# Optimization experiments

Measured on AMD Instinct MI355X. Metric: run time of the kernel, lower is better.

The kernel has to match this reference:

```python
import jax, jax.numpy as jnp
import numpy as np

N_SRC = 50000
N_DST = 50000
E = 800000
IN_DIM = 128
OUT_DIM = 64
HEADS = 4
NEG_SLOPE = 0.2  # PyG GATConv default negative_slope
EPS = 1e-16      # PyG softmax denominator epsilon


def setup_inputs() -> dict:
    key = jax.random.key(0)
    ks = jax.random.split(key, 8)
    x_src = jax.random.normal(ks[0], (N_SRC, IN_DIM), dtype=jnp.float32)
    x_dst = jax.random.normal(ks[1], (N_DST, IN_DIM), dtype=jnp.float32)
    src = jax.random.randint(ks[2], (E,), 0, N_SRC, dtype=jnp.int32)
    dst = jax.random.randint(ks[3], (E,), 0, N_DST, dtype=jnp.int32)
    edge_index = jnp.stack([src, dst], axis=0)
    W_src = jax.random.normal(ks[4], (IN_DIM, HEADS * OUT_DIM), dtype=jnp.float32) / np.sqrt(IN_DIM)
    W_dst = jax.random.normal(ks[5], (IN_DIM, HEADS * OUT_DIM), dtype=jnp.float32) / np.sqrt(IN_DIM)
    att_src = jax.random.normal(ks[6], (HEADS, OUT_DIM), dtype=jnp.float32) / np.sqrt(OUT_DIM)
    att_dst = jax.random.normal(ks[7], (HEADS, OUT_DIM), dtype=jnp.float32) / np.sqrt(OUT_DIM)
    bias = jnp.zeros((OUT_DIM,), dtype=jnp.float32)
    return {"x_src": x_src, "x_dst": x_dst, "edge_index": edge_index,
            "W_src": W_src, "W_dst": W_dst, "att_src": att_src,
            "att_dst": att_dst, "bias": bias}


def reference(x_src, x_dst, edge_index, W_src, W_dst, att_src, att_dst, bias):
    # Linear projections -> [N, H, C]
    hs = (x_src @ W_src).reshape(N_SRC, HEADS, OUT_DIM)
    hd = (x_dst @ W_dst).reshape(N_DST, HEADS, OUT_DIM)
    # Per-node attention logits -> [N, H]
    a_s = jnp.einsum('nhc,hc->nh', hs, att_src)
    a_d = jnp.einsum('nhc,hc->nh', hd, att_dst)

    src, dst = edge_index[0], edge_index[1]
    # Per-edge logits [E, H]
    alpha = jax.nn.leaky_relu(a_s[src] + a_d[dst], negative_slope=NEG_SLOPE)
    # Segment softmax over edges sharing the same dst node
    amax = jax.ops.segment_max(alpha, dst, num_segments=N_DST)
    alpha = jnp.exp(alpha - amax[dst])
    denom = jax.ops.segment_sum(alpha, dst, num_segments=N_DST)
    alpha = alpha / (denom[dst] + EPS)
    # (dropout=0 / eval mode: no attention dropout)
    # Message + scatter-add aggregation: out[i] = sum_e alpha_e * hs[src_e]
    msg = hs[src] * alpha[:, :, None]                 # [E, H, C]
    out = jax.ops.segment_sum(msg, dst, num_segments=N_DST)  # [N_dst, H, C]
    # concat=False -> mean over heads, then bias
    return out.mean(axis=1) + bias
```

## Files before the change

### kernel.cpp

```cpp
#include <hip/hip_runtime.h>
#include <hip/hip_bf16.h>

#define N_SRC 50000
#define N_DST 50000
#define NEDGE 800000
#define IND   128
#define HEADS 4
#define CDIM  64
#define HC    256
#define KTOT  512
#define MAXDEG 96
#define HIST_GPB 256
#define NB_HIST2 2048
#define DPG 6250
#define NB_G16 3125
#define NB_CAST 3125

typedef _Float16 half8  __attribute__((ext_vector_type(8)));
typedef _Float16 half2t __attribute__((ext_vector_type(2)));
typedef float    f32x4  __attribute__((ext_vector_type(4)));
typedef int      i32x4  __attribute__((ext_vector_type(4)));

static __device__ __forceinline__ unsigned int pack2h(float a, float b) {
    union { half2t h; unsigned int u; } v;
    v.h[0] = (_Float16)a; v.h[1] = (_Float16)b;
    return v.u;
}
static __device__ __forceinline__ half2t bits2h(unsigned int u) {
    union { unsigned int u; half2t h; } v; v.u = u; return v.h;
}

__global__ void prep0_kernel(const float* __restrict__ Wdst,
                             const float* __restrict__ att_d,
                             float* __restrict__ WdA,
                             const float* __restrict__ Wsrc,
                             const float* __restrict__ att_s,
                             float* __restrict__ WsA,
                             _Float16* __restrict__ WfT,
                             int* __restrict__ deg) {
    int b = blockIdx.x, tid = threadIdx.x;
    if (b < 196) {
        int i = b * 256 + tid;
        if (i < N_DST) deg[i] = 0;
    } else if (b < 198) {
        int id = (b - 196) * 256 + tid;
        int k = id >> 2, h = id & 3;
        float acc = 0.f;
        for (int c = 0; c < CDIM; ++c)
            acc += Wdst[k * HC + h * CDIM + c] * att_d[h * CDIM + c];
        WdA[id] = acc;
    } else if (b < 200) {
        int id = (b - 198) * 256 + tid;
        int k = id >> 2, h = id & 3;
        float acc = 0.f;
        for (int c = 0; c < CDIM; ++c)
            acc += Wsrc[k * HC + h * CDIM + c] * att_s[h * CDIM + c];
        WsA[id] = acc;
    } else {
        int idx = (b - 200) * 256 + tid;
        int c = idx >> 9, hk = idx & 511;
        int h = hk >> 7, k = hk & 127;
        WfT[idx] = (_Float16)Wsrc[k * HC + h * CDIM + c];
    }
}

__global__ __launch_bounds__(256) void big_kernel(
        const float* __restrict__ x_dst, const float* __restrict__ WdA,
        float* __restrict__ a_d,
        const float* __restrict__ x_src, const float* __restrict__ WsA,
        float* __restrict__ a_s,
        _Float16* __restrict__ xh,
        const int* __restrict__ src, const int* __restrict__ dst,
        int* __restrict__ deg, int* __restrict__ col2) {
    int b = blockIdx.x, tid = threadIdx.x;
    if (b < NB_HIST2) {
        int g  = b & 7;
        int bg = b >> 3;
        int lo = g * DPG, hi = lo + DPG;
        #pragma unroll 1
        for (int it = 0; it < 4; ++it) {
            int base = ((it * HIST_GPB + bg) << 10) + (tid << 2);
            if (base >= NEDGE) break;
            i32x4 dv = __builtin_nontemporal_load((const i32x4*)(dst + base));
            i32x4 sv = __builtin_nontemporal_load((const i32x4*)(src + base));
            #pragma unroll
            for (int j = 0; j < 4; ++j) {
                int d = dv[j];
                if (d >= lo && d < hi) {
                    int r = atomicAdd(&deg[d], 1);
                    if (r < MAXDEG) col2[d * MAXDEG + r] = sv[j];
                }
            }
        }
        return;
    }
    int rank = b - NB_HIST2;
    if (rank < 2 * NB_G16) {
        const float* xbase; const float4* wa; float* outp; int which;
        if (rank < NB_G16) { xbase = x_dst; wa = (const float4*)WdA; outp = a_d; which = rank; }
        else               { xbase = x_src; wa = (const float4*)WsA; outp = a_s; which = rank - NB_G16; }
        int w = tid >> 6, lane = tid & 63;
        float4 wa0 = wa[lane], wa1 = wa[lane + 64];
        int n0 = which * 16 + w * 4;
        #pragma unroll
        for (int p = 0; p < 4; ++p) {
            int n = n0 + p;
            const float* xp = xbase + (size_t)n * IND;
            float x0 = xp[lane], x1 = xp[lane + 64];
            float p0 = x0 * wa0.x + x1 * wa1.x;
            float p1 = x0 * wa0.y + x1 * wa1.y;
            float p2 = x0 * wa0.z + x1 * wa1.z;
            float p3 = x0 * wa0.w + x1 * wa1.w;
            for (int off = 32; off >= 1; off >>= 1) {
                p0 += __shfl_xor(p0, off, 64);
                p1 += __shfl_xor(p1, off, 64);
                p2 += __shfl_xor(p2, off, 64);
                p3 += __shfl_xor(p3, off, 64);
            }
            if (lane == 0) {
                outp[n * 4 + 0] = p0; outp[n * 4 + 1] = p1;
                outp[n * 4 + 2] = p2; outp[n * 4 + 3] = p3;
            }
        }
    } else {
        int e = (rank - 2 * NB_G16) * 256 + tid;
        const float* xp = x_src + (size_t)e * 8;
        float4 u0 = *(const float4*)(xp);
        float4 u1 = *(const float4*)(xp + 4);
        half8 v;
        v[0] = (_Float16)u0.x; v[1] = (_Float16)u0.y;
        v[2] = (_Float16)u0.z; v[3] = (_Float16)u0.w;
        v[4] = (_Float16)u1.x; v[5] = (_Float16)u1.y;
        v[6] = (_Float16)u1.z; v[7] = (_Float16)u1.w;
        *(half8*)(xh + (size_t)e * 8) = v;
    }
}

__global__ __launch_bounds__(256) void aggregate_kernel(
        const int* __restrict__ deg, const int* __restrict__ col2,
        const float4* __restrict__ as4, const float4* __restrict__ ad4,
        const unsigned int* __restrict__ xh32,
        unsigned int* __restrict__ z32) {
    __shared__ int    s_off[4][MAXDEG];
    __shared__ float4 s_w[4][MAXDEG];
    int tid = threadIdx.x;
    int wv = tid >> 6, lane = tid & 63;
    int i = (blockIdx.x * 256 + tid) >> 6;
    if (i >= N_DST) return;
    int dg = deg[i]; if (dg > MAXDEG) dg = MAXDEG;
    unsigned int* zo = z32 + (size_t)i * 256 + lane;
    if (dg == 0) {
        zo[0] = 0u; zo[64] = 0u; zo[128] = 0u; zo[192] = 0u;
        return;
    }
    float4 ad = ad4[i];
    const int* crow = col2 + i * MAXDEG;

    float s0 = 0.f, s1 = 0.f, s2 = 0.f, s3 = 0.f;
    for (int e = lane; e < dg; e += 64) {
        int sn = crow[e];
        float4 av = as4[sn];
        float lx = av.x + ad.x; lx = lx > 0.f ? lx : 0.2f * lx;
        float ly = av.y + ad.y; ly = ly > 0.f ? ly : 0.2f * ly;
        float lz = av.z + ad.z; lz = lz > 0.f ? lz : 0.2f * lz;
        float lw = av.w + ad.w; lw = lw > 0.f ? lw : 0.2f * lw;
        float w0 = __expf(lx), w1 = __expf(ly), w2 = __expf(lz), w3 = __expf(lw);
        s0 += w0; s1 += w1; s2 += w2; s3 += w3;
        s_off[wv][e] = sn;
        s_w[wv][e] = (float4){w0, w1, w2, w3};
    }
    for (int off = 32; off >= 1; off >>= 1) {
        s0 += __shfl_xor(s0, off, 64);
        s1 += __shfl_xor(s1, off, 64);
        s2 += __shfl_xor(s2, off, 64);
        s3 += __shfl_xor(s3, off, 64);
    }
    float i0 = 0.25f / (s0 + 1e-16f);
    float i1 = 0.25f / (s1 + 1e-16f);
    float i2 = 0.25f / (s2 + 1e-16f);
    float i3 = 0.25f / (s3 + 1e-16f);

    for (int e = lane; e < dg; e += 64) {
        float4 wf = s_w[wv][e];
        wf.x *= i0; wf.y *= i1; wf.z *= i2; wf.w *= i3;
        s_w[wv][e] = wf;
    }
    __asm__ volatile("s_waitcnt lgkmcnt(0)" ::: "memory");

    const unsigned int* xb = xh32 + lane;
    float z00 = 0.f, z01 = 0.f, z10 = 0.f, z11 = 0.f;
    float z20 = 0.f, z21 = 0.f, z30 = 0.f, z31 = 0.f;
    int j = 0;
    for (; j + 4 <= dg; j += 4) {
        int sn0 = s_off[wv][j],     sn1 = s_off[wv][j + 1];
        int sn2 = s_off[wv][j + 2], sn3 = s_off[wv][j + 3];
        float4 w0 = s_w[wv][j],     w1 = s_w[wv][j + 1];
        float4 w2 = s_w[wv][j + 2], w3 = s_w[wv][j + 3];
        unsigned int g0 = xb[sn0 << 6];
        unsigned int g1 = xb[sn1 << 6];
        unsigned int g2 = xb[sn2 << 6];
        unsigned int g3 = xb[sn3 << 6];
        half2t hx;
        hx = bits2h(g0);
        { float xa = (float)hx[0], xb2 = (float)hx[1];
          z00 += w0.x * xa; z01 += w0.x * xb2; z10 += w0.y * xa; z11 += w0.y * xb2;
          z20 += w0.z * xa; z21 += w0.z * xb2; z30 += w0.w * xa; z31 += w0.w * xb2; }
        hx = bits2h(g1);
        { float xa = (float)hx[0], xb2 = (float)hx[1];
          z00 += w1.x * xa; z01 += w1.x * xb2; z10 += w1.y * xa; z11 += w1.y * xb2;
          z20 += w1.z * xa; z21 += w1.z * xb2; z30 += w1.w * xa; z31 += w1.w * xb2; }
        hx = bits2h(g2);
        { float xa = (float)hx[0], xb2 = (float)hx[1];
          z00 += w2.x * xa; z01 += w2.x * xb2; z10 += w2.y * xa; z11 += w2.y * xb2;
          z20 += w2.z * xa; z21 += w2.z * xb2; z30 += w2.w * xa; z31 += w2.w * xb2; }
        hx = bits2h(g3);
        { float xa = (float)hx[0], xb2 = (float)hx[1];
          z00 += w3.x * xa; z01 += w3.x * xb2; z10 += w3.y * xa; z11 += w3.y * xb2;
          z20 += w3.z * xa; z21 += w3.z * xb2; z30 += w3.w * xa; z31 += w3.w * xb2; }
    }
    for (; j < dg; ++j) {
        int sn0 = s_off[wv][j];
        float4 w0 = s_w[wv][j];
        unsigned int g0 = xb[sn0 << 6];
        half2t hx = bits2h(g0);
        float xa = (float)hx[0], xb2 = (float)hx[1];
        z00 += w0.x * xa; z01 += w0.x * xb2; z10 += w0.y * xa; z11 += w0.y * xb2;
        z20 += w0.z * xa; z21 += w0.z * xb2; z30 += w0.w * xa; z31 += w0.w * xb2;
    }
    zo[0]   = pack2h(z00, z01);
    zo[64]  = pack2h(z10, z11);
    zo[128] = pack2h(z20, z21);
    zo[192] = pack2h(z30, z31);
}

__global__ __launch_bounds__(256) void fgemm_kernel(
        const _Float16* __restrict__ z, const _Float16* __restrict__ WfT,
        const float* __restrict__ bias, float* __restrict__ out) {
    __shared__ _Float16 sW[64 * KTOT];
    int tid = threadIdx.x;
    {
        const float4* wsrc = (const float4*)WfT;
        #pragma unroll
        for (int it = 0; it < 16; ++it) {
            int idx = it * 256 + tid;
            int row = idx >> 6, slot = idx & 63;
            float4 v = wsrc[idx];
            int byte_off = row * 1024 + ((slot * 16) ^ ((row & 7) << 4));
            *(float4*)((char*)sW + byte_off) = v;
        }
    }

    int w = tid >> 6, lane = tid & 63;
    int ll = lane & 15, q = lane >> 4;
    int rbase = blockIdx.x * 64 + w * 16;

    int arow = rbase + ll;
    if (arow >= N_DST) arow = N_DST - 1;
    const _Float16* zr = z + (size_t)arow * KTOT + q * 8;
    half8 afrag[16];
    #pragma unroll
    for (int s = 0; s < 16; ++s)
        afrag[s] = *(const half8*)(zr + s * 32);

    f32x4 acc[4];
    #pragma unroll
    for (int t = 0; t < 4; ++t) acc[t] = (f32x4){0.f, 0.f, 0.f, 0.f};

    __syncthreads();
    int sw = (ll & 7) << 4;
    #pragma unroll
    for (int t = 0; t < 4; ++t) {
        const char* rowp = (const char*)sW + (t * 16 + ll) * 1024;
        f32x4 c = acc[t];
        #pragma unroll
        for (int s = 0; s < 16; ++s) {
            half8 bb = *(const half8*)(rowp + ((s * 64 + q * 16) ^ sw));
            c = __builtin_amdgcn_mfma_f32_16x16x32_f16(afrag[s], bb, c, 0, 0, 0);
        }
        acc[t] = c;
    }

    #pragma unroll
    for (int t = 0; t < 4; ++t) {
        float bv = bias[t * 16 + ll];
        #pragma unroll
        for (int r = 0; r < 4; ++r) {
            int n = rbase + q * 4 + r;
            if (n < N_DST) out[(size_t)n * CDIM + t * 16 + ll] = acc[t][r] + bv;
        }
    }
}

extern "C" void kernel_launch(void* const* d_in, const int* in_sizes, int n_in,
                              void* d_out, int out_size, void* d_ws, size_t ws_size,
                              hipStream_t stream) {
    const float* x_src   = (const float*)d_in[0];
    const float* x_dst   = (const float*)d_in[1];
    const int*   ei      = (const int*)d_in[2];
    const float* W_src   = (const float*)d_in[3];
    const float* W_dst   = (const float*)d_in[4];
    const float* att_src = (const float*)d_in[5];
    const float* att_dst = (const float*)d_in[6];
    const float* bias    = (const float*)d_in[7];
    float* out = (float*)d_out;

    char* ws = (char*)d_ws;
    _Float16* xh   = (_Float16*)ws; ws += (size_t)N_SRC * IND * 2;
    _Float16* z    = (_Float16*)ws; ws += (size_t)N_DST * KTOT * 2;
    int*    col2   = (int*)ws;    ws += (size_t)N_DST * MAXDEG * 4;
    float*  a_s    = (float*)ws;  ws += (size_t)N_SRC * 4 * 4;
    float*  a_d    = (float*)ws;  ws += (size_t)N_DST * 4 * 4;
    float*  WdA    = (float*)ws;  ws += 2048;
    float*  WsA    = (float*)ws;  ws += 2048;
    _Float16* WfT  = (_Float16*)ws; ws += (size_t)CDIM * KTOT * 2;
    int*    deg    = (int*)ws;    ws += N_DST * 4;

    prep0_kernel<<<328, 256, 0, stream>>>(W_dst, att_dst, WdA,
                                          W_src, att_src, WsA, WfT, deg);
    big_kernel<<<NB_HIST2 + 2 * NB_G16 + NB_CAST, 256, 0, stream>>>(
            x_dst, WdA, a_d, x_src, WsA, a_s, xh,
            ei, ei + NEDGE, deg, col2);
    aggregate_kernel<<<(N_DST + 3) / 4, 256, 0, stream>>>(
            deg, col2, (const float4*)a_s, (const float4*)a_d,
            (const unsigned int*)xh, (unsigned int*)z);
    fgemm_kernel<<<(N_DST + 63) / 64, 256, 0, stream>>>(z, WfT, bias, out);
}
```

Before: 218.2 us.

## Fuse aggregation and final projection GEMM into one kernel via LDS staging

Merges the aggregate and fgemm kernels into one 1024-thread-block kernel. Each of 16 waves aggregates one destination row into a swizzled LDS tile, then 4 waves run the MFMA projection against the weight matrix, which is staged through LDS in two halves. This removes the global round-trip of the fp16 intermediate z (about 51MB written and read) and one kernel launch. In exchange, each block reloads the 64KB weight matrix for only 16 rows, adds several block-wide barriers, and leaves 12 of 16 waves idle during the GEMM phase.

```diff
diff --git a/kernel.cpp b/kernel.cpp
--- a/kernel.cpp
+++ b/kernel.cpp
@@ -15,6 +15,7 @@
 #define DPG 6250
 #define NB_G16 3125
 #define NB_CAST 3125
+#define NB_FUSED 3125
 
 typedef _Float16 half8  __attribute__((ext_vector_type(8)));
 typedef _Float16 half2t __attribute__((ext_vector_type(2)));
@@ -136,157 +137,144 @@
     }
 }
 
-__global__ __launch_bounds__(256) void aggregate_kernel(
+__global__ __launch_bounds__(1024, 4) void aggf_kernel(
         const int* __restrict__ deg, const int* __restrict__ col2,
         const float4* __restrict__ as4, const float4* __restrict__ ad4,
         const unsigned int* __restrict__ xh32,
-        unsigned int* __restrict__ z32) {
-    __shared__ int    s_off[4][MAXDEG];
-    __shared__ float4 s_w[4][MAXDEG];
+        const _Float16* __restrict__ WfT,
+        const float* __restrict__ bias, float* __restrict__ out) {
+    __shared__ char smem[32768];
+    __shared__ char zmem[16384];
+    int* s_off   = (int*)smem;
+    float4* s_w  = (float4*)(smem + 6144);
     int tid = threadIdx.x;
     int wv = tid >> 6, lane = tid & 63;
-    int i = (blockIdx.x * 256 + tid) >> 6;
-    if (i >= N_DST) return;
+    int i = blockIdx.x * 16 + wv;
     int dg = deg[i]; if (dg > MAXDEG) dg = MAXDEG;
-    unsigned int* zo = z32 + (size_t)i * 256 + lane;
+    char* zrow = zmem + wv * 1024;
+    int zswz = (wv & 7) << 4;
+
     if (dg == 0) {
-        zo[0] = 0u; zo[64] = 0u; zo[128] = 0u; zo[192] = 0u;
-        return;
-    }
-    float4 ad = ad4[i];
-    const int* crow = col2 + i * MAXDEG;
-
-    float s0 = 0.f, s1 = 0.f, s2 = 0.f, s3 = 0.f;
-    for (int e = lane; e < dg; e += 64) {
-        int sn = crow[e];
-        float4 av = as4[sn];
-        float lx = av.x + ad.x; lx = lx > 0.f ? lx : 0.2f * lx;
-        float ly = av.y + ad.y; ly = ly > 0.f ? ly : 0.2f * ly;
-        float lz = av.z + ad.z; lz = lz > 0.f ? lz : 0.2f * lz;
-        float lw = av.w + ad.w; lw = lw > 0.f ? lw : 0.2f * lw;
-        float w0 = __expf(lx), w1 = __expf(ly), w2 = __expf(lz), w3 = __expf(lw);
-        s0 += w0; s1 += w1; s2 += w2; s3 += w3;
-        s_off[wv][e] = sn;
-        s_w[wv][e] = (float4){w0, w1, w2, w3};
-    }
-    for (int off = 32; off >= 1; off >>= 1) {
-        s0 += __shfl_xor(s0, off, 64);
-        s1 += __shfl_xor(s1, off, 64);
-        s2 += __shfl_xor(s2, off, 64);
-        s3 += __shfl_xor(s3, off, 64);
-    }
-    float i0 = 0.25f / (s0 + 1e-16f);
-    float i1 = 0.25f / (s1 + 1e-16f);
-    float i2 = 0.25f / (s2 + 1e-16f);
-    float i3 = 0.25f / (s3 + 1e-16f);
-
-    for (int e = lane; e < dg; e += 64) {
-        float4 wf = s_w[wv][e];
-        wf.x *= i0; wf.y *= i1; wf.z *= i2; wf.w *= i3;
-        s_w[wv][e] = wf;
-    }
-    __asm__ volatile("s_waitcnt lgkmcnt(0)" ::: "memory");
-
-    const unsigned int* xb = xh32 + lane;
-    float z00 = 0.f, z01 = 0.f, z10 = 0.f, z11 = 0.f;
-    float z20 = 0.f, z21 = 0.f, z30 = 0.f, z31 = 0.f;
-    int j = 0;
-    for (; j + 4 <= dg; j += 4) {
-        int sn0 = s_off[wv][j],     sn1 = s_off[wv][j + 1];
-        int sn2 = s_off[wv][j + 2], sn3 = s_off[wv][j + 3];
-        float4 w0 = s_w[wv][j],     w1 = s_w[wv][j + 1];
-        float4 w2 = s_w[wv][j + 2], w3 = s_w[wv][j + 3];
-        unsigned int g0 = xb[sn0 << 6];
-        unsigned int g1 = xb[sn1 << 6];
-        unsigned int g2 = xb[sn2 << 6];
-        unsigned int g3 = xb[sn3 << 6];
-        half2t hx;
-        hx = bits2h(g0);
-        { float xa = (float)hx[0], xb2 = (float)hx[1];
-          z00 += w0.x * xa; z01 += w0.x * xb2; z10 += w0.y * xa; z11 += w0.y * xb2;
-          z20 += w0.z * xa; z21 += w0.z * xb2; z30 += w0.w * xa; z31 += w0.w * xb2; }
-        hx = bits2h(g1);
-        { float xa = (float)hx[0], xb2 = (float)hx[1];
-          z00 += w1.x * xa; z01 += w1.x * xb2; z10 += w1.y * xa; z11 += w1.y * xb2;
-          z20 += w1.z * xa; z21 += w1.z * xb2; z30 += w1.w * xa; z31 += w1.w * xb2; }
-        hx = bits2h(g2);
-        { float xa = (float)hx[0], xb2 = (float)hx[1];
-          z00 += w2.x * xa; z01 += w2.x * xb2; z10 += w2.y * xa; z11 += w2.y * xb2;
-          z20 += w2.z * xa; z21 += w2.z * xb2; z30 += w2.w * xa; z31 += w2.w * xb2; }
-        hx = bits2h(g3);
-        { float xa = (float)hx[0], xb2 = (float)hx[1];
-          z00 += w3.x * xa; z01 += w3.x * xb2; z10 += w3.y * xa; z11 += w3.y * xb2;
-          z20 += w3.z * xa; z21 += w3.z * xb2; z30 += w3.w * xa; z31 += w3.w * xb2; }
-    }
-    for (; j < dg; ++j) {
-        int sn0 = s_off[wv][j];
-        float4 w0 = s_w[wv][j];
-        unsigned int g0 = xb[sn0 << 6];
-        half2t hx = bits2h(g0);
-        float xa = (float)hx[0], xb2 = (float)hx[1];
-        z00 += w0.x * xa; z01 += w0.x * xb2; z10 += w0.y * xa; z11 += w0.y * xb2;
-        z20 += w0.z * xa; z21 += w0.z * xb2; z30 += w0.w * xa; z31 += w0.w * xb2;
-    }
-    zo[0]   = pack2h(z00, z01);
-    zo[64]  = pack2h(z10, z11);
-    zo[128] = pack2h(z20, z21);
-    zo[192] = pack2h(z30, z31);
-}
-
-__global__ __launch_bounds__(256) void fgemm_kernel(
-        const _Float16* __restrict__ z, const _Float16* __restrict__ WfT,
-        const float* __restrict__ bias, float* __restrict__ out) {
-    __shared__ _Float16 sW[64 * KTOT];
-    int tid = threadIdx.x;
-    {
-        const float4* wsrc = (const float4*)WfT;
+        *(unsigned int*)(zrow + (((0 * 64 + lane) * 4) ^ zswz)) = 0u;
+        *(unsigned int*)(zrow + (((1 * 64 + lane) * 4) ^ zswz)) = 0u;
+        *(unsigned int*)(zrow + (((2 * 64 + lane) * 4) ^ zswz)) = 0u;
+        *(unsigned int*)(zrow + (((3 * 64 + lane) * 4) ^ zswz)) = 0u;
+    } else {
+        float4 ad = ad4[i];
+        const int* crow = col2 + i * MAXDEG;
+
+        float s0 = 0.f, s1 = 0.f, s2 = 0.f, s3 = 0.f;
+        for (int e = lane; e < dg; e += 64) {
+            int sn = crow[e];
+            float4 av = as4[sn];
+            float lx = av.x + ad.x; lx = lx > 0.f ? lx : 0.2f * lx;
+            float ly = av.y + ad.y; ly = ly > 0.f ? ly : 0.2f * ly;
+            float lz = av.z + ad.z; lz = lz > 0.f ? lz : 0.2f * lz;
+            float lw = av.w + ad.w; lw = lw > 0.f ? lw : 0.2f * lw;
+            float w0 = __expf(lx), w1 = __expf(ly), w2 = __expf(lz), w3 = __expf(lw);
+            s0 += w0; s1 += w1; s2 += w2; s3 += w3;
+            s_off[wv * MAXDEG + e] = sn;
+            s_w[wv * MAXDEG + e] = (float4){w0, w1, w2, w3};
+        }
+        for (int off = 32; off >= 1; off >>= 1) {
+            s0 += __shfl_xor(s0, off, 64);
+            s1 += __shfl_xor(s1, off, 64);
+            s2 += __shfl_xor(s2, off, 64);
+            s3 += __shfl_xor(s3, off, 64);
+        }
+        float i0 = 0.25f / (s0 + 1e-16f);
+        float i1 = 0.25f / (s1 + 1e-16f);
+        float i2 = 0.25f / (s2 + 1e-16f);
+        float i3 = 0.25f / (s3 + 1e-16f);
+        for (int e = lane; e < dg; e += 64) {
+            float4 wf = s_w[wv * MAXDEG + e];
+            wf.x *= i0; wf.y *= i1; wf.z *= i2; wf.w *= i3;
+            s_w[wv * MAXDEG + e] = wf;
+        }
+        __asm__ volatile("s_waitcnt lgkmcnt(0)" ::: "memory");
+
+        const unsigned int* xb = xh32 + lane;
+        float z00 = 0.f, z01 = 0.f, z10 = 0.f, z11 = 0.f;
+        float z20 = 0.f, z21 = 0.f, z30 = 0.f, z31 = 0.f;
+        int j = 0;
+        for (; j + 4 <= dg; j += 4) {
+            int sn0 = s_off[wv * MAXDEG + j],     sn1 = s_off[wv * MAXDEG + j + 1];
+            int sn2 = s_off[wv * MAXDEG + j + 2], sn3 = s_off[wv * MAXDEG + j + 3];
+            float4 w0 = s_w[wv * MAXDEG + j],     w1 = s_w[wv * MAXDEG + j + 1];
+            float4 w2 = s_w[wv * MAXDEG + j + 2], w3 = s_w[wv * MAXDEG + j + 3];
+            unsigned int g0 = xb[sn0 << 6];
+            unsigned int g1 = xb[sn1 << 6];
+            unsigned int g2 = xb[sn2 << 6];
+            unsigned int g3 = xb[sn3 << 6];
+            half2t hx;
+            hx = bits2h(g0);
+            { float xa = (float)hx[0], xc = (float)hx[1];
+              z00 += w0.x * xa; z01 += w0.x * xc; z10 += w0.y * xa; z11 += w0.y * xc;
+              z20 += w0.z * xa; z21 += w0.z * xc; z30 += w0.w * xa; z31 += w0.w * xc; }
+            hx = bits2h(g1);
+            { float xa = (float)hx[0], xc = (float)hx[1];
+              z00 += w1.x * xa; z01 += w1.x * xc; z10 += w1.y * xa; z11 += w1.y * xc;
+              z20 += w1.z * xa; z21 += w1.z * xc; z30 += w1.w * xa; z31 += w1.w * xc; }
+            hx = bits2h(g2);
+            { float xa = (float)hx[0], xc = (float)hx[1];
+              z00 += w2.x * xa; z01 += w2.x * xc; z10 += w2.y * xa; z11 += w2.y * xc;
+              z20 += w2.z * xa; z21 += w2.z * xc; z30 += w2.w * xa; z31 += w2.w * xc; }
+            hx = bits2h(g3);
+            { float xa = (float)hx[0], xc = (float)hx[1];
+              z00 += w3.x * xa; z01 += w3.x * xc; z10 += w3.y * xa; z11 += w3.y * xc;
+              z20 += w3.z * xa; z21 += w3.z * xc; z30 += w3.w * xa; z31 += w3.w * xc; }
+        }
+        for (; j < dg; ++j) {
+            int sn0 = s_off[wv * MAXDEG + j];
+            float4 w0 = s_w[wv * MAXDEG + j];
+            unsigned int g0 = xb[sn0 << 6];
+            half2t hx = bits2h(g0);
+            float xa = (float)hx[0], xc = (float)hx[1];
+            z00 += w0.x * xa; z01 += w0.x * xc; z10 += w0.y * xa; z11 += w0.y * xc;
+            z20 += w0.z * xa; z21 += w0.z * xc; z30 += w0.w * xa; z31 += w0.w * xc;
+        }
+        *(unsigned int*)(zrow + (((0 * 64 + lane) * 4) ^ zswz)) = pack2h(z00, z01);
+        *(unsigned int*)(zrow + (((1 * 64 + lane) * 4) ^ zswz)) = pack2h(z10, z11);
+        *(unsigned int*)(zrow + (((2 * 64 + lane) * 4) ^ zswz)) = pack2h(z20, z21);
+        *(unsigned int*)(zrow + (((3 * 64 + lane) * 4) ^ zswz)) = pack2h(z30, z31);
+    }
+    __syncthreads();
+
+    int ll = lane & 15, q = lane >> 4;
+    int t = wv & 3;
+    int sw = (ll & 7) << 4;
+    f32x4 acc = (f32x4){0.f, 0.f, 0.f, 0.f};
+    const float4* wsrc = (const float4*)WfT;
+    #pragma unroll
+    for (int half = 0; half < 2; ++half) {
         #pragma unroll
-        for (int it = 0; it < 16; ++it) {
-            int idx = it * 256 + tid;
-            int row = idx >> 6, slot = idx & 63;
-            float4 v = wsrc[idx];
-            int byte_off = row * 1024 + ((slot * 16) ^ ((row & 7) << 4));
-            *(float4*)((char*)sW + byte_off) = v;
-        }
-    }
-
-    int w = tid >> 6, lane = tid & 63;
-    int ll = lane & 15, q = lane >> 4;
-    int rbase = blockIdx.x * 64 + w * 16;
-
-    int arow = rbase + ll;
-    if (arow >= N_DST) arow = N_DST - 1;
-    const _Float16* zr = z + (size_t)arow * KTOT + q * 8;
-    half8 afrag[16];
-    #pragma unroll
-    for (int s = 0; s < 16; ++s)
-        afrag[s] = *(const half8*)(zr + s * 32);
-
-    f32x4 acc[4];
-    #pragma unroll
-    for (int t = 0; t < 4; ++t) acc[t] = (f32x4){0.f, 0.f, 0.f, 0.f};
-
-    __syncthreads();
-    int sw = (ll & 7) << 4;
-    #pragma unroll
-    for (int t = 0; t < 4; ++t) {
-        const char* rowp = (const char*)sW + (t * 16 + ll) * 1024;
-        f32x4 c = acc[t];
-        #pragma unroll
-        for (int s = 0; s < 16; ++s) {
-            half8 bb = *(const half8*)(rowp + ((s * 64 + q * 16) ^ sw));
-            c = __builtin_amdgcn_mfma_f32_16x16x32_f16(afrag[s], bb, c, 0, 0, 0);
-        }
-        acc[t] = c;
-    }
-
-    #pragma unroll
-    for (int t = 0; t < 4; ++t) {
+        for (int it = 0; it < 2; ++it) {
+            int idx = it * 1024 + tid;
+            int row = idx >> 5, slot = idx & 31;
+            float4 v = wsrc[row * 64 + half * 32 + slot];
+            *(float4*)(smem + row * 512 + ((slot * 16) ^ ((row & 7) << 4))) = v;
+        }
+        __syncthreads();
+        if (wv < 4) {
+            const char* rowp  = smem + (t * 16 + ll) * 512;
+            const char* zbase = zmem + ll * 1024;
+            #pragma unroll
+            for (int s2 = 0; s2 < 8; ++s2) {
+                int s = half * 8 + s2;
+                half8 a  = *(const half8*)(zbase + ((s * 64 + q * 16) ^ sw));
+                half8 bb = *(const half8*)(rowp + ((s2 * 64 + q * 16) ^ sw));
+                acc = __builtin_amdgcn_mfma_f32_16x16x32_f16(a, bb, acc, 0, 0, 0);
+            }
+        }
+        __syncthreads();
+    }
+    if (wv < 4) {
         float bv = bias[t * 16 + ll];
+        int rbase = blockIdx.x * 16;
         #pragma unroll
         for (int r = 0; r < 4; ++r) {
             int n = rbase + q * 4 + r;
-            if (n < N_DST) out[(size_t)n * CDIM + t * 16 + ll] = acc[t][r] + bv;
+            out[(size_t)n * CDIM + t * 16 + ll] = acc[r] + bv;
         }
     }
 }
@@ -306,7 +294,6 @@
 
     char* ws = (char*)d_ws;
     _Float16* xh   = (_Float16*)ws; ws += (size_t)N_SRC * IND * 2;
-    _Float16* z    = (_Float16*)ws; ws += (size_t)N_DST * KTOT * 2;
     int*    col2   = (int*)ws;    ws += (size_t)N_DST * MAXDEG * 4;
     float*  a_s    = (float*)ws;  ws += (size_t)N_SRC * 4 * 4;
     float*  a_d    = (float*)ws;  ws += (size_t)N_DST * 4 * 4;
@@ -320,8 +307,7 @@
     big_kernel<<<NB_HIST2 + 2 * NB_G16 + NB_CAST, 256, 0, stream>>>(
             x_dst, WdA, a_d, x_src, WsA, a_s, xh,
             ei, ei + NEDGE, deg, col2);
-    aggregate_kernel<<<(N_DST + 3) / 4, 256, 0, stream>>>(
+    aggf_kernel<<<NB_FUSED, 1024, 0, stream>>>(
             deg, col2, (const float4*)a_s, (const float4*)a_d,
-            (const unsigned int*)xh, (unsigned int*)z);
-    fgemm_kernel<<<(N_DST + 63) / 64, 256, 0, stream>>>(z, WfT, bias, out);
-}
+            (const unsigned int*)xh, WfT, bias, out);
+}
```

After: 220.0 us. Within noise of the previous version (+0.8%).
